# Kernel tuning notes

Measured on AMD Instinct MI355X. Metric: run time of the kernel, lower is better.

The kernel has to match this reference:

```python
import jax, jax.numpy as jnp
import numpy as np


def setup_inputs() -> dict:
    key = jax.random.key(0)
    k1, k2, k3 = jax.random.split(key, 3)
    B, H, I, O, Dp1 = 4, 2048, 1024, 1024, 4  # degree=3 -> degree+1=4
    x = jax.random.normal(k1, (B, H, I, Dp1), dtype=jnp.float32)
    weight = 0.1 * jax.random.normal(k2, (O, Dp1), dtype=jnp.float32)
    weighted_sum = 0.1 * jax.random.normal(k3, (O, I), dtype=jnp.float32)
    return {"x": x, "weight": weight, "weighted_sum": weighted_sum}


def reference(x, weight, weighted_sum):
    # Original: weights[o,i,d] = weighted_sum[o,i] * weight[o,d];
    #           out[b,h,o] = sum_{i,d} x[b,h,i,d] * weights[o,i,d]
    # Fused 3-operand einsum avoids materializing the (O, I, D+1) intermediate.
    return jnp.einsum('bhid,oi,od->bho', x, weighted_sum, weight)
```

## Files before the change

kernel.cpp:

```cpp
#include <hip/hip_runtime.h>

typedef unsigned short u16;
typedef u16 u16x4 __attribute__((ext_vector_type(4)));
typedef float f32x4 __attribute__((ext_vector_type(4)));
typedef __bf16 bf16x8 __attribute__((ext_vector_type(8)));

#define M_DIM 8192
#define N_DIM 1024
#define K_DIM 4096

__device__ __forceinline__ u16 f2bf(float f) {
  unsigned u = __float_as_uint(f);
  u += 0x7FFFu + ((u >> 16) & 1u);
  return (u16)(u >> 16);
}

__global__ __launch_bounds__(256) void k_cvt(const float* __restrict__ x,
                                             u16* __restrict__ y) {
  long i = ((long)blockIdx.x * 256 + threadIdx.x) * 4;
  f32x4 a = *(const f32x4*)(x + i);
  u16x4 r;
  r[0] = f2bf(a[0]); r[1] = f2bf(a[1]); r[2] = f2bf(a[2]); r[3] = f2bf(a[3]);
  *(u16x4*)(y + i) = r;
}

__global__ __launch_bounds__(256) void k_w2(const float* __restrict__ w,
                                            const float* __restrict__ ws,
                                            u16* __restrict__ w2) {
  int idx = blockIdx.x * 256 + threadIdx.x;
  int o = idx >> 10;
  float s = ws[idx];
  f32x4 wv = *(const f32x4*)(w + o * 4);
  u16x4 r;
  r[0] = f2bf(s * wv[0]); r[1] = f2bf(s * wv[1]);
  r[2] = f2bf(s * wv[2]); r[3] = f2bf(s * wv[3]);
  *(u16x4*)(w2 + (size_t)idx * 4) = r;
}

typedef __attribute__((address_space(1))) const void gvoid_t;
typedef __attribute__((address_space(3))) void lvoid_t;
__device__ __forceinline__ void gll16(const void* g, void* l) {
  __builtin_amdgcn_global_load_lds((gvoid_t*)g, (lvoid_t*)l, 16, 0, 0);
}

__global__ __launch_bounds__(512) void k_gemm(const u16* __restrict__ A,
                                              const u16* __restrict__ Bt,
                                              float* __restrict__ C) {
  __shared__ u16 sA[128 * 32];
  __shared__ u16 sB[128 * 32];

  const int t    = threadIdx.x;
  const int lane = t & 63;
  const int wid  = t >> 6;
  const int m0   = blockIdx.y * 128;
  const int n0   = blockIdx.x * 128;

  const int row0 = t >> 2;
  const int kc0  = (t & 3) * 8;
  const u16* gA0 = A  + (size_t)(m0 + row0) * K_DIM + kc0;
  const u16* gB0 = Bt + (size_t)(n0 + row0) * K_DIM + kc0;
  u16* lA0 = sA + t * 8;
  u16* lB0 = sB + t * 8;

  const int wm = (wid >> 1) * 32;
  const int wn = (wid & 1) * 64;
  const int fr = lane & 15;
  const int kg = (lane >> 4) * 8;

  f32x4 acc[2][4];
#pragma unroll
  for (int i = 0; i < 2; i++)
#pragma unroll
    for (int j = 0; j < 4; j++) acc[i][j] = (f32x4){0.f, 0.f, 0.f, 0.f};

  for (int k0 = 0; k0 < K_DIM; k0 += 32) {
    gll16(gA0, lA0);
    gll16(gB0, lB0);
    gA0 += 32; gB0 += 32;
    __syncthreads();

    bf16x8 af[2], bf[4];
#pragma unroll
    for (int mi = 0; mi < 2; mi++)
      af[mi] = *(const bf16x8*)(sA + (wm + mi * 16 + fr) * 32 + kg);
#pragma unroll
    for (int ni = 0; ni < 4; ni++)
      bf[ni] = *(const bf16x8*)(sB + (wn + ni * 16 + fr) * 32 + kg);

#pragma unroll
    for (int mi = 0; mi < 2; mi++)
#pragma unroll
      for (int ni = 0; ni < 4; ni++)
        acc[mi][ni] = __builtin_amdgcn_mfma_f32_16x16x32_bf16(
            af[mi], bf[ni], acc[mi][ni], 0, 0, 0);
    __syncthreads();
  }

  const int cr = (lane >> 4) * 4;
  const int cc = lane & 15;
#pragma unroll
  for (int mi = 0; mi < 2; mi++)
#pragma unroll
    for (int ni = 0; ni < 4; ni++) {
      float* cp = C + (size_t)(m0 + wm + mi * 16 + cr) * N_DIM +
                  (n0 + wn + ni * 16 + cc);
#pragma unroll
      for (int r = 0; r < 4; r++) cp[(size_t)r * N_DIM] = acc[mi][ni][r];
    }
}

extern "C" void kernel_launch(void* const* d_in, const int* in_sizes, int n_in,
                              void* d_out, int out_size, void* d_ws, size_t ws_size,
                              hipStream_t stream) {
  const float* x  = (const float*)d_in[0];
  const float* w  = (const float*)d_in[1];
  const float* ws = (const float*)d_in[2];
  float* out = (float*)d_out;

  u16* xbf = (u16*)d_ws;
  u16* w2  = xbf + (size_t)M_DIM * K_DIM;

  k_cvt<<<32768, 256, 0, stream>>>(x, xbf);
  k_w2<<<4096, 256, 0, stream>>>(w, ws, w2);

  dim3 grid(N_DIM / 128, M_DIM / 128);
  k_gemm<<<grid, 512, 0, stream>>>(xbf, w2, out);
}
```

Baseline: 302.1 us.

## Double GEMM K-tile to 64 with XOR-swizzled LDS layout

The GEMM main loop now stages a K-slice of 64 instead of 32 per iteration, so the number of barrier pairs and global-to-LDS issue rounds is halved. Each thread issues two direct global-to-LDS loads per operand. The LDS column chunks are XOR-swizzled by row so the wider 128-byte rows do not produce bank conflicts on the MFMA fragment reads. LDS use doubles to 32 KB per block, which may reduce occupancy, and there is still no double buffering.

```diff
diff --git a/kernel.cpp b/kernel.cpp
--- a/kernel.cpp
+++ b/kernel.cpp
@@ -46,8 +46,8 @@
 __global__ __launch_bounds__(512) void k_gemm(const u16* __restrict__ A,
                                               const u16* __restrict__ Bt,
                                               float* __restrict__ C) {
-  __shared__ u16 sA[128 * 32];
-  __shared__ u16 sB[128 * 32];
+  __shared__ u16 sA[128 * 64];
+  __shared__ u16 sB[128 * 64];
 
   const int t    = threadIdx.x;
   const int lane = t & 63;
@@ -55,17 +55,20 @@
   const int m0   = blockIdx.y * 128;
   const int n0   = blockIdx.x * 128;
 
-  const int row0 = t >> 2;
-  const int kc0  = (t & 3) * 8;
-  const u16* gA0 = A  + (size_t)(m0 + row0) * K_DIM + kc0;
-  const u16* gB0 = Bt + (size_t)(n0 + row0) * K_DIM + kc0;
-  u16* lA0 = sA + t * 8;
-  u16* lB0 = sB + t * 8;
+  const int s0 = t, s1 = t + 512;
+  const int r0 = s0 >> 3, c0 = (s0 & 7) ^ (r0 & 7);
+  const int r1 = s1 >> 3, c1 = (s1 & 7) ^ (r1 & 7);
+  const u16* gA0 = A  + (size_t)(m0 + r0) * K_DIM + c0 * 8;
+  const u16* gA1 = A  + (size_t)(m0 + r1) * K_DIM + c1 * 8;
+  const u16* gB0 = Bt + (size_t)(n0 + r0) * K_DIM + c0 * 8;
+  const u16* gB1 = Bt + (size_t)(n0 + r1) * K_DIM + c1 * 8;
+  u16* lA0 = sA + s0 * 8;  u16* lA1 = sA + s1 * 8;
+  u16* lB0 = sB + s0 * 8;  u16* lB1 = sB + s1 * 8;
 
   const int wm = (wid >> 1) * 32;
   const int wn = (wid & 1) * 64;
   const int fr = lane & 15;
-  const int kg = (lane >> 4) * 8;
+  const int lc = lane >> 4;
 
   f32x4 acc[2][4];
 #pragma unroll
@@ -73,26 +76,34 @@
 #pragma unroll
     for (int j = 0; j < 4; j++) acc[i][j] = (f32x4){0.f, 0.f, 0.f, 0.f};
 
-  for (int k0 = 0; k0 < K_DIM; k0 += 32) {
-    gll16(gA0, lA0);
-    gll16(gB0, lB0);
-    gA0 += 32; gB0 += 32;
+  for (int k0 = 0; k0 < K_DIM; k0 += 64) {
+    gll16(gA0, lA0); gll16(gA1, lA1);
+    gll16(gB0, lB0); gll16(gB1, lB1);
+    gA0 += 64; gA1 += 64; gB0 += 64; gB1 += 64;
     __syncthreads();
 
-    bf16x8 af[2], bf[4];
 #pragma unroll
-    for (int mi = 0; mi < 2; mi++)
-      af[mi] = *(const bf16x8*)(sA + (wm + mi * 16 + fr) * 32 + kg);
+    for (int ks = 0; ks < 2; ks++) {
+      bf16x8 af[2], bf[4];
 #pragma unroll
-    for (int ni = 0; ni < 4; ni++)
-      bf[ni] = *(const bf16x8*)(sB + (wn + ni * 16 + fr) * 32 + kg);
-
+      for (int mi = 0; mi < 2; mi++) {
+        int r  = wm + mi * 16 + fr;
+        int pc = (ks * 4 + lc) ^ (r & 7);
+        af[mi] = *(const bf16x8*)(sA + r * 64 + pc * 8);
+      }
 #pragma unroll
-    for (int mi = 0; mi < 2; mi++)
+      for (int ni = 0; ni < 4; ni++) {
+        int r  = wn + ni * 16 + fr;
+        int pc = (ks * 4 + lc) ^ (r & 7);
+        bf[ni] = *(const bf16x8*)(sB + r * 64 + pc * 8);
+      }
 #pragma unroll
-      for (int ni = 0; ni < 4; ni++)
-        acc[mi][ni] = __builtin_amdgcn_mfma_f32_16x16x32_bf16(
-            af[mi], bf[ni], acc[mi][ni], 0, 0, 0);
+      for (int mi = 0; mi < 2; mi++)
+#pragma unroll
+        for (int ni = 0; ni < 4; ni++)
+          acc[mi][ni] = __builtin_amdgcn_mfma_f32_16x16x32_bf16(
+              af[mi], bf[ni], acc[mi][ni], 0, 0, 0);
+    }
     __syncthreads();
   }
 
```

After: 279.5 us. 1.08x faster.
